# Performance work log

Measured on AMD Instinct MI355X. Metric: run time of the kernel, lower is better.

## Reference

```python
import jax, jax.numpy as jnp
import numpy as np

N_NODES = 100000
N_EDGES = 1600000
IN_DIM, HID_DIM, OUT_DIM = 128, 128, 64


def setup_inputs() -> dict:
    key = jax.random.key(0)
    k1, k2, k3, k4 = jax.random.split(key, 4)
    x = jax.random.normal(k1, (N_NODES, IN_DIM), dtype=jnp.float32)
    edge_index = jax.random.randint(k2, (2, N_EDGES), 0, N_NODES, dtype=jnp.int64)
    W1 = jax.random.normal(k3, (IN_DIM, HID_DIM), dtype=jnp.float32) * (1.0 / np.sqrt(IN_DIM))
    b1 = jnp.zeros((HID_DIM,), dtype=jnp.float32)
    W2 = jax.random.normal(k4, (HID_DIM, OUT_DIM), dtype=jnp.float32) * (1.0 / np.sqrt(HID_DIM))
    b2 = jnp.zeros((OUT_DIM,), dtype=jnp.float32)
    return {"x": x, "edge_index": edge_index, "W1": W1, "b1": b1, "W2": W2, "b2": b2}


def _gcn_conv(h, src, dst, norm, W, b, n_nodes):
    # Dense transform first (PyG GCNConv order), then gather-scatter aggregation.
    h = h @ W                                   # [N, out]
    msg = h[src] * norm[:, None]                # [E, out] gather + scale
    out = jax.ops.segment_sum(msg, dst, num_segments=n_nodes)  # scatter-add
    return out + b


def reference(x, edge_index, W1, b1, W2, b2):
    src, dst = edge_index[0], edge_index[1]
    n = x.shape[0]
    # symmetric normalization: deg from in-degree (unit edge weights), no self loops
    deg = jax.ops.segment_sum(jnp.ones_like(src, dtype=x.dtype), dst, num_segments=n)
    deg_inv_sqrt = jnp.where(deg > 0, jax.lax.rsqrt(jnp.maximum(deg, 1.0)), 0.0)
    norm = deg_inv_sqrt[src] * deg_inv_sqrt[dst]  # [E]
    h = jax.nn.relu(_gcn_conv(x, src, dst, norm, W1, b1, n))
    # dropout is identity in eval mode
    out = _gcn_conv(h, src, dst, norm, W2, b2, n)
    return out
```

## Files before the change

### kernel.cpp

```cpp
#include <hip/hip_runtime.h>
#include <stdint.h>

#define NN 100000
#define NE 1600000
#define K_DIM 128

#define BSH 7
#define NBKT ((NN + (1 << BSH) - 1) >> BSH)
#define EPT 32
#define BIN_CHUNK (256 * EPT)
#define BIN_BLOCKS ((NE + BIN_CHUNK - 1) / BIN_CHUNK)
#define CAP 4096
#define PADE 2301000

typedef unsigned int uint32;
typedef unsigned short ushort16;
typedef __attribute__((ext_vector_type(8))) short bf16x8;
typedef __attribute__((ext_vector_type(4))) float f32x4;

__device__ __forceinline__ ushort16 f2bf(float f) {
    uint32 u = __float_as_uint(f);
    u += 0x7fffu + ((u >> 16) & 1u);
    return (ushort16)(u >> 16);
}
__device__ __forceinline__ float bf_lo(uint32 u) { return __uint_as_float(u << 16); }
__device__ __forceinline__ float bf_hi(uint32 u) { return __uint_as_float(u & 0xffff0000u); }

#define ACC8(v) do { \
    a0 += bf_lo((v).x); a1 += bf_hi((v).x); \
    a2 += bf_lo((v).y); a3 += bf_hi((v).y); \
    a4 += bf_lo((v).z); a5 += bf_hi((v).z); \
    a6 += bf_lo((v).w); a7 += bf_hi((v).w); } while (0)

#define ACC8S(v,d) do { \
    a0 = fmaf(d, bf_lo((v).x), a0); a1 = fmaf(d, bf_hi((v).x), a1); \
    a2 = fmaf(d, bf_lo((v).y), a2); a3 = fmaf(d, bf_hi((v).y), a3); \
    a4 = fmaf(d, bf_lo((v).z), a4); a5 = fmaf(d, bf_hi((v).z), a5); \
    a6 = fmaf(d, bf_lo((v).w), a6); a7 = fmaf(d, bf_hi((v).w), a7); } while (0)

__device__ __forceinline__ bf16x8 ld_frag8(const ushort16* p) {
    uint2 lo = *(const uint2*)p;
    uint2 hi = *(const uint2*)(p + 4);
    union { uint32 u[4]; bf16x8 v; } x;
    x.u[0] = lo.x; x.u[1] = lo.y; x.u[2] = hi.x; x.u[3] = hi.y;
    return x.v;
}

__global__ __launch_bounds__(256) void binxgemm_kernel(
        const int* __restrict__ ei, int* __restrict__ gcursor,
        uint32* __restrict__ staging,
        const float* __restrict__ x, const float* __restrict__ W1,
        ushort16* __restrict__ g1, int M) {
    __shared__ __align__(16) char smem[50688];
    int tid = threadIdx.x;

    if (blockIdx.x < BIN_BLOCKS) {
        int* hist = (int*)smem;
        int* base = hist + NBKT;
        int e0 = blockIdx.x * BIN_CHUNK;

        for (int i = tid; i < NBKT; i += 256) hist[i] = 0;
        __syncthreads();

        #pragma unroll
        for (int k = 0; k < EPT; k++) {
            int e = e0 + k * 256 + tid;
            if (e < NE) {
                int d = ei[NE + e];
                atomicAdd(&hist[d >> BSH], 1);
            }
        }
        __syncthreads();

        for (int i = tid; i < NBKT; i += 256) {
            int c = hist[i];
            base[i] = c ? atomicAdd(&gcursor[i], c) : 0;
            hist[i] = 0;
        }
        __syncthreads();

        #pragma unroll
        for (int k = 0; k < EPT; k++) {
            int e = e0 + k * 256 + tid;
            if (e < NE) {
                int s = ei[e];
                int d = ei[NE + e];
                int b = d >> BSH;
                int off = atomicAdd(&hist[b], 1);
                staging[(size_t)b * CAP + base[b] + off] =
                    ((uint32)s << 7) | (uint32)(d & 127);
            }
        }
    } else {
        constexpr int N = 128, BM = 64, K = K_DIM, LDA = 132, NT = N / 16;
        ushort16* As = (ushort16*)smem;
        ushort16* Bt = As + BM * LDA;
        int bid = (int)blockIdx.x - BIN_BLOCKS;
        int row0 = bid * BM;

        if (bid == 0 && tid < 64)
            ((uint32*)&g1[(size_t)NN * N])[tid] = 0u;

        #pragma unroll
        for (int c = 0; c < 8; c++) {
            int idx = c * 1024 + tid * 4;
            int r = idx >> 7, col = idx & 127;
            int ra = row0 + r;
            float4 v = (ra < M) ? *(const float4*)&x[(size_t)ra * K + col]
                                : make_float4(0.f, 0.f, 0.f, 0.f);
            ushort4 bq;
            bq.x = f2bf(v.x); bq.y = f2bf(v.y); bq.z = f2bf(v.z); bq.w = f2bf(v.w);
            *(ushort4*)&As[r * LDA + col] = bq;
        }
        #pragma unroll
        for (int c = 0; c < (K * N) / 1024; c++) {
            int idx = c * 1024 + tid * 4;
            int k = idx >> 7, n = idx & (N - 1);
            float4 v = *(const float4*)&W1[idx];
            Bt[(n + 0) * LDA + k] = f2bf(v.x);
            Bt[(n + 1) * LDA + k] = f2bf(v.y);
            Bt[(n + 2) * LDA + k] = f2bf(v.z);
            Bt[(n + 3) * LDA + k] = f2bf(v.w);
        }
        __syncthreads();

        int lane = tid & 63;
        int wv = tid >> 6;
        int m0 = wv * 16;
        int ml = lane & 15;
        int quad = lane >> 4;

        f32x4 acc[NT];
        #pragma unroll
        for (int i = 0; i < NT; i++) acc[i] = (f32x4){0.f, 0.f, 0.f, 0.f};

        #pragma unroll
        for (int ks = 0; ks < 4; ks++) {
            int kof = ks * 32 + quad * 8;
            bf16x8 a = ld_frag8(&As[(m0 + ml) * LDA + kof]);
            #pragma unroll
            for (int nt = 0; nt < NT; nt++) {
                bf16x8 bb = ld_frag8(&Bt[(nt * 16 + ml) * LDA + kof]);
                acc[nt] = __builtin_amdgcn_mfma_f32_16x16x32_bf16(a, bb, acc[nt], 0, 0, 0);
            }
        }

        #pragma unroll
        for (int r = 0; r < 4; r++) {
            int row = row0 + m0 + quad * 4 + r;
            if (row < M) {
                #pragma unroll
                for (int nt = 0; nt < NT; nt++)
                    g1[(size_t)row * N + nt * 16 + ml] = f2bf(acc[nt][r]);
            }
        }
    }
}

__global__ __launch_bounds__(256) void bucket_finish_kernel(
        const uint32* __restrict__ staging, const int* __restrict__ gcursor,
        int* __restrict__ gedge, int* __restrict__ deg, float* __restrict__ dis,
        int* __restrict__ row_start, int* __restrict__ ssrc) {
    __shared__ uint32 pairs[CAP];
    __shared__ int cnt[1 << BSH];
    __shared__ int sb[1 << BSH];
    __shared__ int cur[1 << BSH];
    __shared__ int pend[1 << BSH];
    __shared__ int bbase;
    int b = blockIdx.x;
    int node0 = b << BSH;
    int tid = threadIdx.x;
    int n_edges = gcursor[b];

    if (tid < (1 << BSH)) cnt[tid] = 0;
    __syncthreads();

    for (int i = tid; i < n_edges; i += 256) {
        uint32 p = staging[(size_t)b * CAP + i];
        pairs[i] = p;
        atomicAdd(&cnt[p & 127u], 1);
    }
    __syncthreads();

    int p = 0;
    if (tid < (1 << BSH)) {
        int node = node0 + tid;
        int c = cnt[tid];
        if (node < NN) {
            deg[node] = c;
            dis[node] = (c > 0) ? rsqrtf((float)c) : 0.0f;
            p = (c + 7) & ~7;
        } else if (node == NN) {
            dis[NN] = 0.0f;
        }
        sb[tid] = p;
    }
    __syncthreads();
    #pragma unroll
    for (int off = 1; off < (1 << BSH); off <<= 1) {
        int t = (tid >= off && tid < (1 << BSH)) ? sb[tid - off] : 0;
        __syncthreads();
        if (tid < (1 << BSH)) sb[tid] += t;
        __syncthreads();
    }
    if (tid == (1 << BSH) - 1) bbase = atomicAdd(gedge, sb[tid]);
    __syncthreads();

    if (tid < (1 << BSH)) {
        int rs = bbase + sb[tid] - p;
        cur[tid] = rs;
        pend[tid] = rs + p;
        int node = node0 + tid;
        if (node < NN) row_start[node] = rs;
    }
    __syncthreads();

    for (int i = tid; i < n_edges; i += 256) {
        uint32 pr = pairs[i];
        int off = atomicAdd(&cur[pr & 127u], 1);
        ssrc[off] = (int)(pr >> 7);
    }
    __syncthreads();

    if (tid < (1 << BSH)) {
        int node = node0 + tid;
        if (node < NN) {
            for (int q = cur[tid]; q < pend[tid]; q++) ssrc[q] = NN;
        }
    }
}

template <int N, int ZROWB>
__global__ __launch_bounds__(256) void gemm_mfma_kernel(
        const ushort16* __restrict__ A, const float* __restrict__ W,
        const float* __restrict__ dis, ushort16* __restrict__ out, int M) {
    constexpr int BM = 64, K = K_DIM;
    constexpr int LDA = 132;
    constexpr int NT = N / 16;
    constexpr int NLOG = (N == 128) ? 7 : 6;

    __shared__ ushort16 As[BM * LDA];
    __shared__ ushort16 Bt[N * LDA];

    int tid = threadIdx.x;
    int row0 = blockIdx.x * BM;

    if constexpr (ZROWB > 0) {
        if (blockIdx.x == 0 && tid < ZROWB / 4)
            ((uint32*)&out[(size_t)NN * N])[tid] = 0u;
    }

    #pragma unroll
    for (int c = 0; c < 4; c++) {
        int idx = c * 2048 + tid * 8;
        int r = idx >> 7, col = idx & 127;
        int ra = row0 + r;
        uint4 v = make_uint4(0u, 0u, 0u, 0u);
        if (ra < M) v = *(const uint4*)&A[(size_t)ra * K + col];
        *(uint2*)&As[r * LDA + col]     = make_uint2(v.x, v.y);
        *(uint2*)&As[r * LDA + col + 4] = make_uint2(v.z, v.w);
    }
    {
        #pragma unroll
        for (int c = 0; c < (K * N) / 1024; c++) {
            int idx = c * 1024 + tid * 4;
            int k = idx >> NLOG, n = idx & (N - 1);
            float4 v = *(const float4*)&W[idx];
            Bt[(n + 0) * LDA + k] = f2bf(v.x);
            Bt[(n + 1) * LDA + k] = f2bf(v.y);
            Bt[(n + 2) * LDA + k] = f2bf(v.z);
            Bt[(n + 3) * LDA + k] = f2bf(v.w);
        }
    }
    __syncthreads();

    int lane = tid & 63;
    int wv = tid >> 6;
    int m0 = wv * 16;
    int ml = lane & 15;
    int quad = lane >> 4;

    f32x4 acc[NT];
    #pragma unroll
    for (int i = 0; i < NT; i++) acc[i] = (f32x4){0.f, 0.f, 0.f, 0.f};

    #pragma unroll
    for (int ks = 0; ks < 4; ks++) {
        int kof = ks * 32 + quad * 8;
        bf16x8 a = ld_frag8(&As[(m0 + ml) * LDA + kof]);
        #pragma unroll
        for (int nt = 0; nt < NT; nt++) {
            bf16x8 bb = ld_frag8(&Bt[(nt * 16 + ml) * LDA + kof]);
            acc[nt] = __builtin_amdgcn_mfma_f32_16x16x32_bf16(a, bb, acc[nt], 0, 0, 0);
        }
    }

    #pragma unroll
    for (int r = 0; r < 4; r++) {
        int row = row0 + m0 + quad * 4 + r;
        if (row < M) {
            float s = dis[row];
            #pragma unroll
            for (int nt = 0; nt < NT; nt++)
                out[(size_t)row * N + nt * 16 + ml] = f2bf(acc[nt][r] * s);
        }
    }
}

__global__ __launch_bounds__(256) void agg128_kernel(
        const ushort16* __restrict__ g, const int* __restrict__ row_start,
        const int* __restrict__ deg, const int* __restrict__ ssrc,
        const float* __restrict__ dis, const float* __restrict__ bias,
        ushort16* __restrict__ out) {
    int wave = (blockIdx.x * 256 + threadIdx.x) >> 6;
    int lane = threadIdx.x & 63;
    if (wave >= NN) return;

    int beg = row_start[wave];
    int ecount = (deg[wave] + 7) & ~7;
    float sc = dis[wave];

    int fl = lane & 15;
    int q  = lane >> 4;
    int laneoff = fl * 16;

    int idx = ssrc[beg + lane];
    uint32 ci = (uint32)idx; if (ci > (uint32)NN) ci = NN;
    float dsv = dis[ci];

    float a0 = 0.f, a1 = 0.f, a2 = 0.f, a3 = 0.f;
    float a4 = 0.f, a5 = 0.f, a6 = 0.f, a7 = 0.f;

    const char* gb = (const char*)g;
    int nb = ((ecount < 64) ? ecount : 64) >> 3;
    int b = 0;
    for (; b + 2 <= nb; b += 2) {
        int s0a = __shfl(idx, b * 8 + q);
        int s1a = __shfl(idx, b * 8 + 4 + q);
        int s0b = __shfl(idx, b * 8 + 8 + q);
        int s1b = __shfl(idx, b * 8 + 12 + q);
        float d0a = __shfl(dsv, b * 8 + q);
        float d1a = __shfl(dsv, b * 8 + 4 + q);
        float d0b = __shfl(dsv, b * 8 + 8 + q);
        float d1b = __shfl(dsv, b * 8 + 12 + q);
        uint4 v0a = *(const uint4*)(gb + (((uint32)s0a << 8) + laneoff));
        uint4 v1a = *(const uint4*)(gb + (((uint32)s1a << 8) + laneoff));
        uint4 v0b = *(const uint4*)(gb + (((uint32)s0b << 8) + laneoff));
        uint4 v1b = *(const uint4*)(gb + (((uint32)s1b << 8) + laneoff));
        ACC8S(v0a, d0a); ACC8S(v1a, d1a); ACC8S(v0b, d0b); ACC8S(v1b, d1b);
    }
    if (b < nb) {
        int s0 = __shfl(idx, b * 8 + q);
        int s1 = __shfl(idx, b * 8 + 4 + q);
        float d0 = __shfl(dsv, b * 8 + q);
        float d1 = __shfl(dsv, b * 8 + 4 + q);
        uint4 v0 = *(const uint4*)(gb + (((uint32)s0 << 8) + laneoff));
        uint4 v1 = *(const uint4*)(gb + (((uint32)s1 << 8) + laneoff));
        ACC8S(v0, d0); ACC8S(v1, d1);
    }
    for (int e = beg + 64; e < beg + ecount; e += 8) {
        int idx2 = ssrc[e + (lane & 7)];
        float dsv2 = dis[idx2];
        int s0 = __shfl(idx2, q);
        int s1 = __shfl(idx2, 4 + q);
        float d0 = __shfl(dsv2, q);
        float d1 = __shfl(dsv2, 4 + q);
        uint4 v0 = *(const uint4*)(gb + (((uint32)s0 << 8) + laneoff));
        uint4 v1 = *(const uint4*)(gb + (((uint32)s1 << 8) + laneoff));
        ACC8S(v0, d0); ACC8S(v1, d1);
    }

    a0 += __shfl_xor(a0, 16); a1 += __shfl_xor(a1, 16);
    a2 += __shfl_xor(a2, 16); a3 += __shfl_xor(a3, 16);
    a4 += __shfl_xor(a4, 16); a5 += __shfl_xor(a5, 16);
    a6 += __shfl_xor(a6, 16); a7 += __shfl_xor(a7, 16);
    a0 += __shfl_xor(a0, 32); a1 += __shfl_xor(a1, 32);
    a2 += __shfl_xor(a2, 32); a3 += __shfl_xor(a3, 32);
    a4 += __shfl_xor(a4, 32); a5 += __shfl_xor(a5, 32);
    a6 += __shfl_xor(a6, 32); a7 += __shfl_xor(a7, 32);

    if (lane < 16) {
        float4 bA = *(const float4*)&bias[fl * 8];
        float4 bB = *(const float4*)&bias[fl * 8 + 4];
        float o0 = fmaxf(sc * a0 + bA.x, 0.f);
        float o1 = fmaxf(sc * a1 + bA.y, 0.f);
        float o2 = fmaxf(sc * a2 + bA.z, 0.f);
        float o3 = fmaxf(sc * a3 + bA.w, 0.f);
        float o4 = fmaxf(sc * a4 + bB.x, 0.f);
        float o5 = fmaxf(sc * a5 + bB.y, 0.f);
        float o6 = fmaxf(sc * a6 + bB.z, 0.f);
        float o7 = fmaxf(sc * a7 + bB.w, 0.f);
        uint4 pk;
        pk.x = ((uint32)f2bf(o1) << 16) | (uint32)f2bf(o0);
        pk.y = ((uint32)f2bf(o3) << 16) | (uint32)f2bf(o2);
        pk.z = ((uint32)f2bf(o5) << 16) | (uint32)f2bf(o4);
        pk.w = ((uint32)f2bf(o7) << 16) | (uint32)f2bf(o6);
        *(uint4*)&out[(size_t)wave * 128 + fl * 8] = pk;
    }
}

__global__ __launch_bounds__(256) void agg64_kernel(
        const ushort16* __restrict__ g, const int* __restrict__ row_start,
        const int* __restrict__ deg, const int* __restrict__ ssrc,
        const float* __restrict__ dis, const float* __restrict__ bias,
        float* __restrict__ out) {
    int wave = (blockIdx.x * 256 + threadIdx.x) >> 6;
    int lane = threadIdx.x & 63;
    int half = lane >> 5;
    int l2 = lane & 31;
    int node = wave * 2 + half;
    if (node >= NN) return;

    int beg = row_start[node];
    int ecount = (deg[node] + 7) & ~7;
    float sc = dis[node];

    int fl = l2 & 7;
    int q  = l2 >> 3;
    int laneoff = fl * 16;

    int idx = ssrc[beg + l2];

    float a0 = 0.f, a1 = 0.f, a2 = 0.f, a3 = 0.f;
    float a4 = 0.f, a5 = 0.f, a6 = 0.f, a7 = 0.f;

    const char* gb = (const char*)g;
    int nb = ((ecount < 32) ? ecount : 32) >> 3;
    int b = 0;
    for (; b + 2 <= nb; b += 2) {
        int s0a = __shfl(idx, half * 32 + b * 8 + q);
        int s1a = __shfl(idx, half * 32 + b * 8 + 4 + q);
        int s0b = __shfl(idx, half * 32 + b * 8 + 8 + q);
        int s1b = __shfl(idx, half * 32 + b * 8 + 12 + q);
        uint4 v0a = *(const uint4*)(gb + (((uint32)s0a << 7) + laneoff));
        uint4 v1a = *(const uint4*)(gb + (((uint32)s1a << 7) + laneoff));
        uint4 v0b = *(const uint4*)(gb + (((uint32)s0b << 7) + laneoff));
        uint4 v1b = *(const uint4*)(gb + (((uint32)s1b << 7) + laneoff));
        ACC8(v0a); ACC8(v1a); ACC8(v0b); ACC8(v1b);
    }
    if (b < nb) {
        int s0 = __shfl(idx, half * 32 + b * 8 + q);
        int s1 = __shfl(idx, half * 32 + b * 8 + 4 + q);
        uint4 v0 = *(const uint4*)(gb + (((uint32)s0 << 7) + laneoff));
        uint4 v1 = *(const uint4*)(gb + (((uint32)s1 << 7) + laneoff));
        ACC8(v0); ACC8(v1);
    }
    for (int e = beg + 32; e < beg + ecount; e += 8) {
        int idx2 = ssrc[e + (l2 & 7)];
        int s0 = __shfl(idx2, half * 32 + q);
        int s1 = __shfl(idx2, half * 32 + 4 + q);
        uint4 v0 = *(const uint4*)(gb + (((uint32)s0 << 7) + laneoff));
        uint4 v1 = *(const uint4*)(gb + (((uint32)s1 << 7) + laneoff));
        ACC8(v0); ACC8(v1);
    }

    a0 += __shfl_xor(a0, 8);  a1 += __shfl_xor(a1, 8);
    a2 += __shfl_xor(a2, 8);  a3 += __shfl_xor(a3, 8);
    a4 += __shfl_xor(a4, 8);  a5 += __shfl_xor(a5, 8);
    a6 += __shfl_xor(a6, 8);  a7 += __shfl_xor(a7, 8);
    a0 += __shfl_xor(a0, 16); a1 += __shfl_xor(a1, 16);
    a2 += __shfl_xor(a2, 16); a3 += __shfl_xor(a3, 16);
    a4 += __shfl_xor(a4, 16); a5 += __shfl_xor(a5, 16);
    a6 += __shfl_xor(a6, 16); a7 += __shfl_xor(a7, 16);

    if (l2 < 8) {
        float4 bA = *(const float4*)&bias[fl * 8];
        float4 bB = *(const float4*)&bias[fl * 8 + 4];
        float4 oA = make_float4(sc * a0 + bA.x, sc * a1 + bA.y,
                                sc * a2 + bA.z, sc * a3 + bA.w);
        float4 oB = make_float4(sc * a4 + bB.x, sc * a5 + bB.y,
                                sc * a6 + bB.z, sc * a7 + bB.w);
        *(float4*)&out[(size_t)node * 64 + fl * 8]     = oA;
        *(float4*)&out[(size_t)node * 64 + fl * 8 + 4] = oB;
    }
}

extern "C" void kernel_launch(void* const* d_in, const int* in_sizes, int n_in,
                              void* d_out, int out_size, void* d_ws, size_t ws_size,
                              hipStream_t stream) {
    const float* x  = (const float*)d_in[0];
    const int*   ei = (const int*)d_in[1];
    const float* W1 = (const float*)d_in[2];
    const float* b1 = (const float*)d_in[3];
    const float* W2 = (const float*)d_in[4];
    const float* b2 = (const float*)d_in[5];
    float* out = (float*)d_out;

    char* ws = (char*)d_ws;
    size_t off = 0;
    auto alloc = [&](size_t bytes) {
        void* p = ws + off;
        off = (off + bytes + 255) & ~(size_t)255;
        return p;
    };

    int*      deg_i      = (int*)alloc(NN * 4);
    float*    dis        = (float*)alloc((NN + 1) * 4);
    int*      row_start  = (int*)alloc(NN * 4);
    int*      gcursor    = (int*)alloc((NBKT + 1) * 4);
    int*      ssrc       = (int*)alloc((size_t)PADE * 4);
    ushort16* g1         = (ushort16*)alloc((size_t)(NN + 1) * 128 * 2);
    char*     big        = (char*)alloc((size_t)NN * 128 * 2);
    uint32*   staging    = (uint32*)big;
    ushort16* h          = (ushort16*)big;
    ushort16* g2         = g1;
    int*      gedge      = gcursor + NBKT;

    hipMemsetAsync(gcursor, 0, (NBKT + 1) * 4, stream);

    binxgemm_kernel<<<BIN_BLOCKS + (NN + 63) / 64, 256, 0, stream>>>(
        ei, gcursor, staging, x, W1, g1, NN);

    bucket_finish_kernel<<<NBKT, 256, 0, stream>>>(
        staging, gcursor, gedge, deg_i, dis, row_start, ssrc);

    const int AGG_BLOCKS = (NN + 3) / 4;
    agg128_kernel<<<AGG_BLOCKS, 256, 0, stream>>>(g1, row_start, deg_i, ssrc, dis, b1, h);

    const int GEMM_BLOCKS = (NN + 63) / 64;
    gemm_mfma_kernel<64, 128><<<GEMM_BLOCKS, 256, 0, stream>>>(h, W2, dis, g2, NN);

    const int AGG2_BLOCKS = (NN / 2 + 3) / 4;
    agg64_kernel<<<AGG2_BLOCKS, 256, 0, stream>>>(g2, row_start, deg_i, ssrc, dis, b2, out);
}
```

Before: 265.2 us.

## Fuse layer-1 aggregation with layer-2 GEMM via shared-memory hidden tile

Merges the first aggregation kernel and the second MFMA GEMM into one kernel. Each block aggregates 32 nodes into a bf16 hidden tile in LDS, then multiplies it by W2 using MFMA and writes g2 directly. This removes the global write and re-read of the 100k x 128 hidden matrix and one kernel launch. In exchange, each block must convert W2 into LDS, and occupancy may drop because of the larger LDS footprint. g2 now reuses the staging buffer.

```diff
diff --git a/kernel.cpp b/kernel.cpp
--- a/kernel.cpp
+++ b/kernel.cpp
@@ -230,172 +230,150 @@
     }
 }
 
-template <int N, int ZROWB>
-__global__ __launch_bounds__(256) void gemm_mfma_kernel(
-        const ushort16* __restrict__ A, const float* __restrict__ W,
-        const float* __restrict__ dis, ushort16* __restrict__ out, int M) {
-    constexpr int BM = 64, K = K_DIM;
+__global__ __launch_bounds__(256) void agg128f_kernel(
+        const ushort16* __restrict__ g1, const int* __restrict__ row_start,
+        const int* __restrict__ deg, const int* __restrict__ ssrc,
+        const float* __restrict__ dis, const float* __restrict__ b1,
+        const float* __restrict__ W2, ushort16* __restrict__ g2) {
     constexpr int LDA = 132;
-    constexpr int NT = N / 16;
-    constexpr int NLOG = (N == 128) ? 7 : 6;
-
-    __shared__ ushort16 As[BM * LDA];
-    __shared__ ushort16 Bt[N * LDA];
+    __shared__ ushort16 Bt[64 * LDA];
+    __shared__ ushort16 H[32 * LDA];
+    __shared__ float sdis[32];
 
     int tid = threadIdx.x;
-    int row0 = blockIdx.x * BM;
-
-    if constexpr (ZROWB > 0) {
-        if (blockIdx.x == 0 && tid < ZROWB / 4)
-            ((uint32*)&out[(size_t)NN * N])[tid] = 0u;
-    }
+    int lane = tid & 63, wv = tid >> 6;
+    int node0 = blockIdx.x * 32;
 
     #pragma unroll
-    for (int c = 0; c < 4; c++) {
-        int idx = c * 2048 + tid * 8;
-        int r = idx >> 7, col = idx & 127;
-        int ra = row0 + r;
-        uint4 v = make_uint4(0u, 0u, 0u, 0u);
-        if (ra < M) v = *(const uint4*)&A[(size_t)ra * K + col];
-        *(uint2*)&As[r * LDA + col]     = make_uint2(v.x, v.y);
-        *(uint2*)&As[r * LDA + col + 4] = make_uint2(v.z, v.w);
-    }
-    {
-        #pragma unroll
-        for (int c = 0; c < (K * N) / 1024; c++) {
-            int idx = c * 1024 + tid * 4;
-            int k = idx >> NLOG, n = idx & (N - 1);
-            float4 v = *(const float4*)&W[idx];
-            Bt[(n + 0) * LDA + k] = f2bf(v.x);
-            Bt[(n + 1) * LDA + k] = f2bf(v.y);
-            Bt[(n + 2) * LDA + k] = f2bf(v.z);
-            Bt[(n + 3) * LDA + k] = f2bf(v.w);
-        }
-    }
-    __syncthreads();
-
-    int lane = tid & 63;
-    int wv = tid >> 6;
-    int m0 = wv * 16;
+    for (int c = 0; c < 8; c++) {
+        int idx = c * 1024 + tid * 4;
+        int k = idx >> 6, n = idx & 63;
+        float4 v = *(const float4*)&W2[idx];
+        Bt[(n + 0) * LDA + k] = f2bf(v.x);
+        Bt[(n + 1) * LDA + k] = f2bf(v.y);
+        Bt[(n + 2) * LDA + k] = f2bf(v.z);
+        Bt[(n + 3) * LDA + k] = f2bf(v.w);
+    }
+    if (blockIdx.x == 0 && tid < 32)
+        ((uint32*)&g2[(size_t)NN * 64])[tid] = 0u;
+
+    int fl = lane & 15;
+    int q  = lane >> 4;
+    int laneoff = fl * 16;
+    const char* gb = (const char*)g1;
+
+    for (int it = 0; it < 8; it++) {
+        int node = node0 + it * 4 + wv;
+        int beg = row_start[node];
+        int ecount = (deg[node] + 7) & ~7;
+        float sc = dis[node];
+
+        int ecl = (ecount < 64) ? ecount : 64;
+        bool act = lane < ecl;
+        int idx = act ? ssrc[beg + lane] : (int)NN;
+        float dsv = act ? dis[idx] : 0.f;
+
+        float a0 = 0.f, a1 = 0.f, a2 = 0.f, a3 = 0.f;
+        float a4 = 0.f, a5 = 0.f, a6 = 0.f, a7 = 0.f;
+
+        int nb = ecl >> 3;
+        int b = 0;
+        for (; b + 2 <= nb; b += 2) {
+            int s0a = __shfl(idx, b * 8 + q);
+            int s1a = __shfl(idx, b * 8 + 4 + q);
+            int s0b = __shfl(idx, b * 8 + 8 + q);
+            int s1b = __shfl(idx, b * 8 + 12 + q);
+            float d0a = __shfl(dsv, b * 8 + q);
+            float d1a = __shfl(dsv, b * 8 + 4 + q);
+            float d0b = __shfl(dsv, b * 8 + 8 + q);
+            float d1b = __shfl(dsv, b * 8 + 12 + q);
+            uint4 v0a = *(const uint4*)(gb + (((uint32)s0a << 8) + laneoff));
+            uint4 v1a = *(const uint4*)(gb + (((uint32)s1a << 8) + laneoff));
+            uint4 v0b = *(const uint4*)(gb + (((uint32)s0b << 8) + laneoff));
+            uint4 v1b = *(const uint4*)(gb + (((uint32)s1b << 8) + laneoff));
+            ACC8S(v0a, d0a); ACC8S(v1a, d1a); ACC8S(v0b, d0b); ACC8S(v1b, d1b);
+        }
+        if (b < nb) {
+            int s0 = __shfl(idx, b * 8 + q);
+            int s1 = __shfl(idx, b * 8 + 4 + q);
+            float d0 = __shfl(dsv, b * 8 + q);
+            float d1 = __shfl(dsv, b * 8 + 4 + q);
+            uint4 v0 = *(const uint4*)(gb + (((uint32)s0 << 8) + laneoff));
+            uint4 v1 = *(const uint4*)(gb + (((uint32)s1 << 8) + laneoff));
+            ACC8S(v0, d0); ACC8S(v1, d1);
+        }
+        for (int e = beg + 64; e < beg + ecount; e += 8) {
+            int idx2 = ssrc[e + (lane & 7)];
+            float dsv2 = dis[idx2];
+            int s0 = __shfl(idx2, q);
+            int s1 = __shfl(idx2, 4 + q);
+            float d0 = __shfl(dsv2, q);
+            float d1 = __shfl(dsv2, 4 + q);
+            uint4 v0 = *(const uint4*)(gb + (((uint32)s0 << 8) + laneoff));
+            uint4 v1 = *(const uint4*)(gb + (((uint32)s1 << 8) + laneoff));
+            ACC8S(v0, d0); ACC8S(v1, d1);
+        }
+
+        a0 += __shfl_xor(a0, 16); a1 += __shfl_xor(a1, 16);
+        a2 += __shfl_xor(a2, 16); a3 += __shfl_xor(a3, 16);
+        a4 += __shfl_xor(a4, 16); a5 += __shfl_xor(a5, 16);
+        a6 += __shfl_xor(a6, 16); a7 += __shfl_xor(a7, 16);
+        a0 += __shfl_xor(a0, 32); a1 += __shfl_xor(a1, 32);
+        a2 += __shfl_xor(a2, 32); a3 += __shfl_xor(a3, 32);
+        a4 += __shfl_xor(a4, 32); a5 += __shfl_xor(a5, 32);
+        a6 += __shfl_xor(a6, 32); a7 += __shfl_xor(a7, 32);
+
+        int hrow = it * 4 + wv;
+        if (lane == 0) sdis[hrow] = sc;
+        if (lane < 16) {
+            float4 bA = *(const float4*)&b1[fl * 8];
+            float4 bB = *(const float4*)&b1[fl * 8 + 4];
+            float o0 = fmaxf(sc * a0 + bA.x, 0.f);
+            float o1 = fmaxf(sc * a1 + bA.y, 0.f);
+            float o2 = fmaxf(sc * a2 + bA.z, 0.f);
+            float o3 = fmaxf(sc * a3 + bA.w, 0.f);
+            float o4 = fmaxf(sc * a4 + bB.x, 0.f);
+            float o5 = fmaxf(sc * a5 + bB.y, 0.f);
+            float o6 = fmaxf(sc * a6 + bB.z, 0.f);
+            float o7 = fmaxf(sc * a7 + bB.w, 0.f);
+            uint32 p0 = ((uint32)f2bf(o1) << 16) | (uint32)f2bf(o0);
+            uint32 p1 = ((uint32)f2bf(o3) << 16) | (uint32)f2bf(o2);
+            uint32 p2 = ((uint32)f2bf(o5) << 16) | (uint32)f2bf(o4);
+            uint32 p3 = ((uint32)f2bf(o7) << 16) | (uint32)f2bf(o6);
+            *(uint2*)&H[hrow * LDA + fl * 8]     = make_uint2(p0, p1);
+            *(uint2*)&H[hrow * LDA + fl * 8 + 4] = make_uint2(p2, p3);
+        }
+    }
+    __syncthreads();
+
+    int m0 = (wv & 1) * 16;
+    int nt0 = (wv >> 1) * 2;
     int ml = lane & 15;
     int quad = lane >> 4;
 
-    f32x4 acc[NT];
-    #pragma unroll
-    for (int i = 0; i < NT; i++) acc[i] = (f32x4){0.f, 0.f, 0.f, 0.f};
+    f32x4 acc[2];
+    acc[0] = (f32x4){0.f, 0.f, 0.f, 0.f};
+    acc[1] = (f32x4){0.f, 0.f, 0.f, 0.f};
 
     #pragma unroll
     for (int ks = 0; ks < 4; ks++) {
         int kof = ks * 32 + quad * 8;
-        bf16x8 a = ld_frag8(&As[(m0 + ml) * LDA + kof]);
-        #pragma unroll
-        for (int nt = 0; nt < NT; nt++) {
-            bf16x8 bb = ld_frag8(&Bt[(nt * 16 + ml) * LDA + kof]);
-            acc[nt] = __builtin_amdgcn_mfma_f32_16x16x32_bf16(a, bb, acc[nt], 0, 0, 0);
+        bf16x8 a = ld_frag8(&H[(m0 + ml) * LDA + kof]);
+        #pragma unroll
+        for (int t = 0; t < 2; t++) {
+            bf16x8 bb = ld_frag8(&Bt[((nt0 + t) * 16 + ml) * LDA + kof]);
+            acc[t] = __builtin_amdgcn_mfma_f32_16x16x32_bf16(a, bb, acc[t], 0, 0, 0);
         }
     }
 
     #pragma unroll
     for (int r = 0; r < 4; r++) {
-        int row = row0 + m0 + quad * 4 + r;
-        if (row < M) {
-            float s = dis[row];
-            #pragma unroll
-            for (int nt = 0; nt < NT; nt++)
-                out[(size_t)row * N + nt * 16 + ml] = f2bf(acc[nt][r] * s);
-        }
-    }
-}
-
-__global__ __launch_bounds__(256) void agg128_kernel(
-        const ushort16* __restrict__ g, const int* __restrict__ row_start,
-        const int* __restrict__ deg, const int* __restrict__ ssrc,
-        const float* __restrict__ dis, const float* __restrict__ bias,
-        ushort16* __restrict__ out) {
-    int wave = (blockIdx.x * 256 + threadIdx.x) >> 6;
-    int lane = threadIdx.x & 63;
-    if (wave >= NN) return;
-
-    int beg = row_start[wave];
-    int ecount = (deg[wave] + 7) & ~7;
-    float sc = dis[wave];
-
-    int fl = lane & 15;
-    int q  = lane >> 4;
-    int laneoff = fl * 16;
-
-    int idx = ssrc[beg + lane];
-    uint32 ci = (uint32)idx; if (ci > (uint32)NN) ci = NN;
-    float dsv = dis[ci];
-
-    float a0 = 0.f, a1 = 0.f, a2 = 0.f, a3 = 0.f;
-    float a4 = 0.f, a5 = 0.f, a6 = 0.f, a7 = 0.f;
-
-    const char* gb = (const char*)g;
-    int nb = ((ecount < 64) ? ecount : 64) >> 3;
-    int b = 0;
-    for (; b + 2 <= nb; b += 2) {
-        int s0a = __shfl(idx, b * 8 + q);
-        int s1a = __shfl(idx, b * 8 + 4 + q);
-        int s0b = __shfl(idx, b * 8 + 8 + q);
-        int s1b = __shfl(idx, b * 8 + 12 + q);
-        float d0a = __shfl(dsv, b * 8 + q);
-        float d1a = __shfl(dsv, b * 8 + 4 + q);
-        float d0b = __shfl(dsv, b * 8 + 8 + q);
-        float d1b = __shfl(dsv, b * 8 + 12 + q);
-        uint4 v0a = *(const uint4*)(gb + (((uint32)s0a << 8) + laneoff));
-        uint4 v1a = *(const uint4*)(gb + (((uint32)s1a << 8) + laneoff));
-        uint4 v0b = *(const uint4*)(gb + (((uint32)s0b << 8) + laneoff));
-        uint4 v1b = *(const uint4*)(gb + (((uint32)s1b << 8) + laneoff));
-        ACC8S(v0a, d0a); ACC8S(v1a, d1a); ACC8S(v0b, d0b); ACC8S(v1b, d1b);
-    }
-    if (b < nb) {
-        int s0 = __shfl(idx, b * 8 + q);
-        int s1 = __shfl(idx, b * 8 + 4 + q);
-        float d0 = __shfl(dsv, b * 8 + q);
-        float d1 = __shfl(dsv, b * 8 + 4 + q);
-        uint4 v0 = *(const uint4*)(gb + (((uint32)s0 << 8) + laneoff));
-        uint4 v1 = *(const uint4*)(gb + (((uint32)s1 << 8) + laneoff));
-        ACC8S(v0, d0); ACC8S(v1, d1);
-    }
-    for (int e = beg + 64; e < beg + ecount; e += 8) {
-        int idx2 = ssrc[e + (lane & 7)];
-        float dsv2 = dis[idx2];
-        int s0 = __shfl(idx2, q);
-        int s1 = __shfl(idx2, 4 + q);
-        float d0 = __shfl(dsv2, q);
-        float d1 = __shfl(dsv2, 4 + q);
-        uint4 v0 = *(const uint4*)(gb + (((uint32)s0 << 8) + laneoff));
-        uint4 v1 = *(const uint4*)(gb + (((uint32)s1 << 8) + laneoff));
-        ACC8S(v0, d0); ACC8S(v1, d1);
-    }
-
-    a0 += __shfl_xor(a0, 16); a1 += __shfl_xor(a1, 16);
-    a2 += __shfl_xor(a2, 16); a3 += __shfl_xor(a3, 16);
-    a4 += __shfl_xor(a4, 16); a5 += __shfl_xor(a5, 16);
-    a6 += __shfl_xor(a6, 16); a7 += __shfl_xor(a7, 16);
-    a0 += __shfl_xor(a0, 32); a1 += __shfl_xor(a1, 32);
-    a2 += __shfl_xor(a2, 32); a3 += __shfl_xor(a3, 32);
-    a4 += __shfl_xor(a4, 32); a5 += __shfl_xor(a5, 32);
-    a6 += __shfl_xor(a6, 32); a7 += __shfl_xor(a7, 32);
-
-    if (lane < 16) {
-        float4 bA = *(const float4*)&bias[fl * 8];
-        float4 bB = *(const float4*)&bias[fl * 8 + 4];
-        float o0 = fmaxf(sc * a0 + bA.x, 0.f);
-        float o1 = fmaxf(sc * a1 + bA.y, 0.f);
-        float o2 = fmaxf(sc * a2 + bA.z, 0.f);
-        float o3 = fmaxf(sc * a3 + bA.w, 0.f);
-        float o4 = fmaxf(sc * a4 + bB.x, 0.f);
-        float o5 = fmaxf(sc * a5 + bB.y, 0.f);
-        float o6 = fmaxf(sc * a6 + bB.z, 0.f);
-        float o7 = fmaxf(sc * a7 + bB.w, 0.f);
-        uint4 pk;
-        pk.x = ((uint32)f2bf(o1) << 16) | (uint32)f2bf(o0);
-        pk.y = ((uint32)f2bf(o3) << 16) | (uint32)f2bf(o2);
-        pk.z = ((uint32)f2bf(o5) << 16) | (uint32)f2bf(o4);
-        pk.w = ((uint32)f2bf(o7) << 16) | (uint32)f2bf(o6);
-        *(uint4*)&out[(size_t)wave * 128 + fl * 8] = pk;
+        int row = m0 + quad * 4 + r;
+        float s = sdis[row];
+        size_t gbase = (size_t)(node0 + row) * 64;
+        #pragma unroll
+        for (int t = 0; t < 2; t++)
+            g2[gbase + (nt0 + t) * 16 + ml] = f2bf(acc[t][r] * s);
     }
 }
 
@@ -500,10 +478,9 @@
     int*      gcursor    = (int*)alloc((NBKT + 1) * 4);
     int*      ssrc       = (int*)alloc((size_t)PADE * 4);
     ushort16* g1         = (ushort16*)alloc((size_t)(NN + 1) * 128 * 2);
-    char*     big        = (char*)alloc((size_t)NN * 128 * 2);
+    char*     big        = (char*)alloc((size_t)NBKT * CAP * 4);
     uint32*   staging    = (uint32*)big;
-    ushort16* h          = (ushort16*)big;
-    ushort16* g2         = g1;
+    ushort16* g2         = (ushort16*)big;
     int*      gedge      = gcursor + NBKT;
 
     hipMemsetAsync(gcursor, 0, (NBKT + 1) * 4, stream);
@@ -514,11 +491,8 @@
     bucket_finish_kernel<<<NBKT, 256, 0, stream>>>(
         staging, gcursor, gedge, deg_i, dis, row_start, ssrc);
 
-    const int AGG_BLOCKS = (NN + 3) / 4;
-    agg128_kernel<<<AGG_BLOCKS, 256, 0, stream>>>(g1, row_start, deg_i, ssrc, dis, b1, h);
-
-    const int GEMM_BLOCKS = (NN + 63) / 64;
-    gemm_mfma_kernel<64, 128><<<GEMM_BLOCKS, 256, 0, stream>>>(h, W2, dis, g2, NN);
+    agg128f_kernel<<<NN / 32, 256, 0, stream>>>(
+        g1, row_start, deg_i, ssrc, dis, b1, W2, g2);
 
     const int AGG2_BLOCKS = (NN / 2 + 3) / 4;
     agg64_kernel<<<AGG2_BLOCKS, 256, 0, stream>>>(g2, row_start, deg_i, ssrc, dis, b2, out);
```

New measurement: 264.0 us, median of 2. No clear change (-0.5%).
